# Optimization experiments

Measured on AMD Instinct MI355X. Metric: run time of the kernel, lower is better.

Reference implementation:

```python
import math
import jax, jax.numpy as jnp
import numpy as np

V_NODES = 100000
N_EDGES = 1600000
EMBED = 768
HID = 256
H = 4
FH = HID // H
L = 2
PE_D = EMBED // 4  # 192
SLOPE = 0.2


def make_pe(max_len, d):
    pos = np.arange(max_len, dtype=np.float32)[:, None]
    div = np.exp(np.arange(0, d, 2, dtype=np.float32) * (-math.log(10000.0) / d))
    pe = np.zeros((max_len, d), dtype=np.float32)
    pe[:, 0::2] = np.sin(pos * div)
    pe[:, 1::2] = np.cos(pos * div)
    return jnp.asarray(pe)


def setup_inputs() -> dict:
    key = jax.random.key(0)
    ks = jax.random.split(key, 24)

    def xavier(k, shape):
        fan_in, fan_out = shape[0], shape[1]
        lim = math.sqrt(6.0 / (fan_in + fan_out))
        return jax.random.uniform(k, shape, jnp.float32, -lim, lim)

    in_proj_dim = EMBED + 2 * PE_D  # 1152
    inp = {
        'row_idx': jax.random.randint(ks[0], (V_NODES,), 0, 256),
        'col_idx': jax.random.randint(ks[1], (V_NODES,), 0, 64),
        'edge_index': jax.random.randint(ks[2], (2, N_EDGES), 0, V_NODES),
        'edge_weight': jax.random.uniform(ks[3], (N_EDGES,), jnp.float32),
        'W_in': xavier(ks[4], (in_proj_dim, HID)),
        'b_in': jnp.zeros((HID,), jnp.float32),
        'ln_g': jnp.ones((HID,), jnp.float32),
        'ln_b': jnp.zeros((HID,), jnp.float32),
        'Wq': jnp.stack([xavier(ks[5 + i], (HID, HID)) for i in range(L)]),
        'bq': jnp.zeros((L, HID), jnp.float32),
        'Wk': jnp.stack([xavier(ks[7 + i], (HID, HID)) for i in range(L)]),
        'bk': jnp.zeros((L, HID), jnp.float32),
        'Wv': jnp.stack([xavier(ks[9 + i], (HID, HID)) for i in range(L)]),
        'bv': jnp.zeros((L, HID), jnp.float32),
        'Wo': jnp.stack([xavier(ks[11 + i], (HID, HID)) for i in range(L)]),
        'bo': jnp.zeros((L, HID), jnp.float32),
        'We': jnp.stack([xavier(ks[13 + i], (1, H)) for i in range(L)]),  # edge_proj weight [1,H]
        'be': jnp.zeros((L, H), jnp.float32),
    }
    return inp


def gat_layer(h, src, tgt, ew, Wq, bq, Wk, bk, Wv, bv, Wo, bo, We, be):
    V = h.shape[0]
    Q = (h @ Wq + bq).reshape(V, H, FH)
    K = (h @ Wk + bk).reshape(V, H, FH)
    Vo = (h @ Wv + bv).reshape(V, H, FH)
    # edge bias: Linear(1,H) on edge_weight, then leaky relu -> [E,H]
    edge_bias = jax.nn.leaky_relu(ew[:, None] * We.reshape(1, H) + be, SLOPE)
    attn_raw = jnp.sum(Q[src] * K[tgt], axis=-1) / math.sqrt(FH) + edge_bias  # [E,H]
    attn_exp = jnp.exp(attn_raw)
    deg = jax.ops.segment_sum(attn_exp, tgt, num_segments=V) + 1e-16  # [V,H]
    attn_norm = attn_exp / deg[tgt]  # [E,H] (dropout is identity at eval)
    msg = Vo[src] * attn_norm[:, :, None] * ew[:, None, None]  # [E,H,FH]
    out = jax.ops.segment_sum(msg, tgt, num_segments=V).reshape(V, H * FH)
    return jax.nn.leaky_relu(out @ Wo + bo, SLOPE)


def reference(row_idx, col_idx, edge_index, edge_weight,
              W_in, b_in, ln_g, ln_b,
              Wq, bq, Wk, bk, Wv, bv, Wo, bo, We, be):
    V = row_idx.shape[0]
    row_pe = make_pe(256, PE_D)
    col_pe = make_pe(64, PE_D)
    cell = jnp.zeros((V, EMBED), jnp.float32)  # cell_embeds are zeros in source
    h = jnp.concatenate([cell, row_pe[row_idx], col_pe[col_idx]], axis=-1)
    # input_proj: Linear -> LayerNorm -> ReLU (dropout identity)
    h = h @ W_in + b_in
    mu = jnp.mean(h, axis=-1, keepdims=True)
    var = jnp.var(h, axis=-1, keepdims=True)
    h = (h - mu) / jnp.sqrt(var + 1e-5) * ln_g + ln_b
    h = jax.nn.relu(h)
    src, tgt = edge_index[0], edge_index[1]
    for i in range(L):
        h = gat_layer(h, src, tgt, edge_weight,
                      Wq[i], bq[i], Wk[i], bk[i], Wv[i], bv[i],
                      Wo[i], bo[i], We[i], be[i])
    return h
```

## Files before the change

### kernel.cpp

```cpp
#include <hip/hip_runtime.h>
#include <hip/hip_bf16.h>
#include <type_traits>
#include <math.h>

typedef __attribute__((ext_vector_type(8))) short bf16x8;
typedef __attribute__((ext_vector_type(4))) float f32x4;

typedef __attribute__((address_space(3))) char       lds_char;
typedef const __attribute__((address_space(1))) char g_char;

__device__ __forceinline__ float bf2f(unsigned int u16) {
    union { unsigned int i; float f; } x; x.i = (u16 & 0xffffu) << 16; return x.f;
}
__device__ __forceinline__ unsigned int f2bf(float f) {
    union { float f; unsigned int i; } x; x.f = f;
    unsigned int i = x.i;
    unsigned int r = i + 0x7fffu + ((i >> 16) & 1u);
    return r >> 16;
}

#define SLOPE 0.2f

__global__ void k_hist(const int* __restrict__ tgt, int* __restrict__ cnt, int E) {
    int i = blockIdx.x * blockDim.x + threadIdx.x;
    if (i < E) atomicAdd(&cnt[tgt[i]], 1);
}

__global__ void __launch_bounds__(1024) k_scan1(const int* __restrict__ in, int* __restrict__ out,
                                                int* __restrict__ bsums, int n) {
    __shared__ int sm[1024];
    int i = blockIdx.x * 1024 + threadIdx.x;
    int v = (i < n) ? in[i] : 0;
    sm[threadIdx.x] = v; __syncthreads();
    for (int ofs = 1; ofs < 1024; ofs <<= 1) {
        int t = (threadIdx.x >= ofs) ? sm[threadIdx.x - ofs] : 0;
        __syncthreads();
        sm[threadIdx.x] += t;
        __syncthreads();
    }
    if (i < n) out[i] = sm[threadIdx.x];
    if (threadIdx.x == 1023) bsums[blockIdx.x] = sm[1023];
}

__global__ void __launch_bounds__(1024) k_scan2(int* bsums, int nb) {
    __shared__ int sm[1024];
    int v = (threadIdx.x < nb) ? bsums[threadIdx.x] : 0;
    sm[threadIdx.x] = v; __syncthreads();
    for (int ofs = 1; ofs < 1024; ofs <<= 1) {
        int t = (threadIdx.x >= ofs) ? sm[threadIdx.x - ofs] : 0;
        __syncthreads();
        sm[threadIdx.x] += t;
        __syncthreads();
    }
    if (threadIdx.x < nb) bsums[threadIdx.x] = sm[threadIdx.x] - v;
}

__global__ void __launch_bounds__(1024) k_scan3(int* __restrict__ out1, const int* __restrict__ bsums,
                                                int* __restrict__ off0, int n) {
    int i = blockIdx.x * 1024 + threadIdx.x;
    if (i < n) out1[i] += bsums[blockIdx.x];
    if (i == 0) off0[0] = 0;
}

__global__ void k_scatter(const int* __restrict__ ei, const float* __restrict__ ew,
                          const int* __restrict__ off, int* __restrict__ fill,
                          int2* __restrict__ p, int E) {
    int e = blockIdx.x * blockDim.x + threadIdx.x;
    if (e < E) {
        int s = ei[e], t = ei[E + e];
        int pos = off[t] + atomicAdd(&fill[t], 1);
        p[pos] = make_int2(s, __float_as_int(ew[e]));
    }
}

__global__ void __launch_bounds__(256) k_prep(const float* __restrict__ Wq, const float* __restrict__ Wk,
                                              const float* __restrict__ Wv, const float* __restrict__ Wo,
                                              unsigned short* __restrict__ WT,
                                              const float* __restrict__ bq, const float* __restrict__ bk,
                                              const float* __restrict__ bv, const float* __restrict__ bo,
                                              float* __restrict__ biasF,
                                              const float* __restrict__ W_in, float* __restrict__ AB,
                                              const int* __restrict__ ri, const int* __restrict__ ci,
                                              int* __restrict__ combo, int V) {
    __shared__ float sm[64][65];
    int blk = blockIdx.x;
    int tid = threadIdx.x;
    if (blk < 128) {
        int m = blk >> 4, t = blk & 15;
        int tr = t >> 2, tc = t & 3;
        const float* srcs[4] = {Wq, Wk, Wv, Wo};
        const float* W = srcs[m & 3] + (size_t)(m >> 2) * 65536;
        for (int i = tid; i < 4096; i += 256) {
            int r = i >> 6, c = i & 63;
            sm[r][c] = W[(size_t)(tr * 64 + r) * 256 + tc * 64 + c];
        }
        __syncthreads();
        for (int i = tid; i < 4096; i += 256) {
            int n = i >> 6, k = i & 63;
            WT[(size_t)(m * 256 + tc * 64 + n) * 256 + tr * 64 + k] = (unsigned short)f2bf(sm[k][n]);
        }
    } else if (blk < 136) {
        int m = blk - 128;
        const float* srcs[4] = {bq, bk, bv, bo};
        biasF[m * 256 + tid] = srcs[m & 3][(m >> 2) * 256 + tid];
    } else if (blk < 456) {
        int b2 = blk - 136;
        bool isA = b2 < 256;
        int pos = isA ? b2 : b2 - 256;
        const float* Wb = W_in + (size_t)(isA ? 768 : 960) * 256;
        float* pe = &sm[0][0];
        if (tid < 192) {
            float div = expf(-(float)(tid & ~1) * (logf(10000.0f) / 192.0f));
            float ang = (float)pos * div;
            pe[tid] = (tid & 1) ? cosf(ang) : sinf(ang);
        }
        __syncthreads();
        float acc = 0.f;
        #pragma unroll 8
        for (int d = 0; d < 192; ++d) acc = fmaf(pe[d], Wb[d * 256 + tid], acc);
        AB[b2 * 256 + tid] = acc;
    } else {
        int v = (blk - 456) * 256 + tid;
        if (v < V) combo[v] = ri[v] * 64 + ci[v];
    }
}

__global__ void __launch_bounds__(256) k_h0(const float* __restrict__ AB, const float* __restrict__ b_in,
                                            const float* __restrict__ g, const float* __restrict__ b,
                                            unsigned short* __restrict__ h0t) {
    int wid = threadIdx.x >> 6, lane = threadIdx.x & 63;
    int m = blockIdx.x * 4 + wid;
    int r = m >> 6, c = m & 63;
    float4 a  = ((const float4*)(AB + (size_t)r * 256))[lane];
    float4 bb = ((const float4*)(AB + (size_t)(256 + c) * 256))[lane];
    float4 bi = ((const float4*)b_in)[lane];
    float x0 = a.x + bb.x + bi.x, x1 = a.y + bb.y + bi.y;
    float x2 = a.z + bb.z + bi.z, x3 = a.w + bb.w + bi.w;
    float s = x0 + x1 + x2 + x3;
    #pragma unroll
    for (int msk = 1; msk < 64; msk <<= 1) s += __shfl_xor(s, msk);
    float mu = s * (1.f / 256.f);
    float d0 = x0 - mu, d1 = x1 - mu, d2 = x2 - mu, d3 = x3 - mu;
    float sq = d0 * d0 + d1 * d1 + d2 * d2 + d3 * d3;
    #pragma unroll
    for (int msk = 1; msk < 64; msk <<= 1) sq += __shfl_xor(sq, msk);
    float rstd = rsqrtf(sq * (1.f / 256.f) + 1e-5f);
    float4 gv = ((const float4*)g)[lane], bv = ((const float4*)b)[lane];
    float y0 = fmaxf(fmaf(d0 * rstd, gv.x, bv.x), 0.f);
    float y1 = fmaxf(fmaf(d1 * rstd, gv.y, bv.y), 0.f);
    float y2 = fmaxf(fmaf(d2 * rstd, gv.z, bv.z), 0.f);
    float y3 = fmaxf(fmaf(d3 * rstd, gv.w, bv.w), 0.f);
    uint2 o;
    o.x = f2bf(y0) | (f2bf(y1) << 16);
    o.y = f2bf(y2) | (f2bf(y3) << 16);
    *(uint2*)(h0t + (size_t)m * 256 + lane * 4) = o;
}

template <typename TC, bool LEAKY>
__global__ void __launch_bounds__(256) k_mm(const unsigned short* __restrict__ A,
                                            const unsigned short* __restrict__ WT,
                                            const float* __restrict__ bias,
                                            TC* __restrict__ C, int M, int ldc) {
    __shared__ __align__(16) char AsB[16384];
    __shared__ __align__(16) char BsB[16384];
    int tid = threadIdx.x;
    int R0 = blockIdx.x * 128, C0 = blockIdx.y * 128;
    int lane = tid & 63, wave = tid >> 6;
    int wr = (wave >> 1) * 64, wc = (wave & 1) * 64;
    int fr = lane & 15, fq = lane >> 4;
    f32x4 acc[4][4] = {};
    for (int k0 = 0; k0 < 256; k0 += 64) {
        #pragma unroll
        for (int it = 0; it < 4; ++it) {
            int chunk = it * 256 + tid;
            int r = chunk >> 3, cb = (chunk & 7) * 16;
            int sc = cb ^ ((r & 7) << 4);
            int gr = R0 + r;
            if (gr < M)
                __builtin_amdgcn_global_load_lds(
                    (g_char*)((const char*)(A + (size_t)gr * 256 + k0) + sc),
                    (lds_char*)(AsB + (size_t)(it * 256 + wave * 64) * 16), 16, 0, 0);
            __builtin_amdgcn_global_load_lds(
                (g_char*)((const char*)(WT + (size_t)(C0 + r) * 256 + k0) + sc),
                (lds_char*)(BsB + (size_t)(it * 256 + wave * 64) * 16), 16, 0, 0);
        }
        __syncthreads();
        #pragma unroll
        for (int ks = 0; ks < 2; ++ks) {
            bf16x8 af[4], bfv[4];
            #pragma unroll
            for (int mi = 0; mi < 4; ++mi) {
                int r = wr + mi * 16 + fr;
                int kb = ks * 64 + fq * 16;
                af[mi] = *(const bf16x8*)(AsB + r * 128 + (kb ^ ((r & 7) << 4)));
            }
            #pragma unroll
            for (int ni = 0; ni < 4; ++ni) {
                int r = wc + ni * 16 + fr;
                int kb = ks * 64 + fq * 16;
                bfv[ni] = *(const bf16x8*)(BsB + r * 128 + (kb ^ ((r & 7) << 4)));
            }
            #pragma unroll
            for (int mi = 0; mi < 4; ++mi)
                #pragma unroll
                for (int ni = 0; ni < 4; ++ni)
                    acc[mi][ni] = __builtin_amdgcn_mfma_f32_16x16x32_bf16(af[mi], bfv[ni], acc[mi][ni], 0, 0, 0);
        }
        __syncthreads();
    }
    #pragma unroll
    for (int mi = 0; mi < 4; ++mi) {
        #pragma unroll
        for (int r = 0; r < 4; ++r) {
            int row = R0 + wr + mi * 16 + fq * 4 + r;
            if (row >= M) continue;
            #pragma unroll
            for (int ni = 0; ni < 4; ++ni) {
                int col = C0 + wc + ni * 16 + fr;
                float v = acc[mi][ni][r] + bias[col];
                if (LEAKY) v = fmaxf(v, SLOPE * v);
                if constexpr (std::is_same<TC, float>::value) {
                    C[(size_t)row * ldc + col] = v;
                } else {
                    C[(size_t)row * ldc + col] = (unsigned short)f2bf(v);
                }
            }
        }
    }
}

template <bool USE_COMBO>
__global__ void __launch_bounds__(256) k_edge(const int* __restrict__ off, const int2* __restrict__ pedge,
                                              const int* __restrict__ combo,
                                              const unsigned short* __restrict__ QKV,
                                              const float* __restrict__ We_l, const float* __restrict__ be_l,
                                              unsigned short* __restrict__ out, int V) {
    int wid = threadIdx.x >> 6, lane = threadIdx.x & 63;
    int t = blockIdx.x * 4 + wid;
    if (t >= V) return;
    int q = lane & 15, quarter = lane >> 4;
    int h = q >> 2;
    int krow = USE_COMBO ? combo[t] : t;
    uint4 ka = *(const uint4*)(QKV + (size_t)krow * 768 + 256 + q * 16);
    uint4 kb = *(const uint4*)(QKV + (size_t)krow * 768 + 256 + q * 16 + 8);
    float kf[16];
    kf[0] = bf2f(ka.x); kf[1] = bf2f(ka.x >> 16); kf[2] = bf2f(ka.y); kf[3] = bf2f(ka.y >> 16);
    kf[4] = bf2f(ka.z); kf[5] = bf2f(ka.z >> 16); kf[6] = bf2f(ka.w); kf[7] = bf2f(ka.w >> 16);
    kf[8] = bf2f(kb.x); kf[9] = bf2f(kb.x >> 16); kf[10] = bf2f(kb.y); kf[11] = bf2f(kb.y >> 16);
    kf[12] = bf2f(kb.z); kf[13] = bf2f(kb.z >> 16); kf[14] = bf2f(kb.w); kf[15] = bf2f(kb.w >> 16);
    float Weh = We_l[h], beh = be_l[h];
    float n[16];
    #pragma unroll
    for (int j = 0; j < 16; ++j) n[j] = 0.f;
    float den = 0.f;
    int beg = off[t], end = off[t + 1];
    for (int e0 = beg; e0 < end; e0 += 64) {
        int nrem = end - e0; if (nrem > 64) nrem = 64;
        int sv = 0; float wv = 0.f;
        if (lane < nrem) {
            int2 pr = pedge[e0 + lane];
            sv = pr.x;
            wv = __int_as_float(pr.y);
            if (USE_COMBO) sv = combo[sv];
        }
        for (int i = 0; i < nrem; i += 4) {
            int ei = i + quarter;
            bool act = ei < nrem;
            int eidx = act ? ei : (nrem - 1);
            int srow = __shfl(sv, eidx);
            float w  = __shfl(wv, eidx);
            const unsigned short* base = QKV + (size_t)srow * 768 + q * 16;
            uint4 qa = *(const uint4*)base;
            uint4 qb = *(const uint4*)(base + 8);
            uint4 va = *(const uint4*)(base + 512);
            uint4 vb = *(const uint4*)(base + 520);
            float p;
            p = bf2f(qa.x) * kf[0];
            p = fmaf(bf2f(qa.x >> 16), kf[1], p);
            p = fmaf(bf2f(qa.y),       kf[2], p);
            p = fmaf(bf2f(qa.y >> 16), kf[3], p);
            p = fmaf(bf2f(qa.z),       kf[4], p);
            p = fmaf(bf2f(qa.z >> 16), kf[5], p);
            p = fmaf(bf2f(qa.w),       kf[6], p);
            p = fmaf(bf2f(qa.w >> 16), kf[7], p);
            p = fmaf(bf2f(qb.x),       kf[8], p);
            p = fmaf(bf2f(qb.x >> 16), kf[9], p);
            p = fmaf(bf2f(qb.y),       kf[10], p);
            p = fmaf(bf2f(qb.y >> 16), kf[11], p);
            p = fmaf(bf2f(qb.z),       kf[12], p);
            p = fmaf(bf2f(qb.z >> 16), kf[13], p);
            p = fmaf(bf2f(qb.w),       kf[14], p);
            p = fmaf(bf2f(qb.w >> 16), kf[15], p);
            p += __shfl_xor(p, 1);
            p += __shfl_xor(p, 2);
            float bias = fmaf(w, Weh, beh);
            bias = fmaxf(bias, SLOPE * bias);
            float ex = act ? __expf(fmaf(p, 0.125f, bias)) : 0.f;
            den += ex;
            float cc = ex * w;
            n[0]  = fmaf(cc, bf2f(va.x),       n[0]);
            n[1]  = fmaf(cc, bf2f(va.x >> 16), n[1]);
            n[2]  = fmaf(cc, bf2f(va.y),       n[2]);
            n[3]  = fmaf(cc, bf2f(va.y >> 16), n[3]);
            n[4]  = fmaf(cc, bf2f(va.z),       n[4]);
            n[5]  = fmaf(cc, bf2f(va.z >> 16), n[5]);
            n[6]  = fmaf(cc, bf2f(va.w),       n[6]);
            n[7]  = fmaf(cc, bf2f(va.w >> 16), n[7]);
            n[8]  = fmaf(cc, bf2f(vb.x),       n[8]);
            n[9]  = fmaf(cc, bf2f(vb.x >> 16), n[9]);
            n[10] = fmaf(cc, bf2f(vb.y),       n[10]);
            n[11] = fmaf(cc, bf2f(vb.y >> 16), n[11]);
            n[12] = fmaf(cc, bf2f(vb.z),       n[12]);
            n[13] = fmaf(cc, bf2f(vb.z >> 16), n[13]);
            n[14] = fmaf(cc, bf2f(vb.w),       n[14]);
            n[15] = fmaf(cc, bf2f(vb.w >> 16), n[15]);
        }
    }
    den += __shfl_xor(den, 16);
    den += __shfl_xor(den, 32);
    #pragma unroll
    for (int j = 0; j < 16; ++j) {
        n[j] += __shfl_xor(n[j], 16);
        n[j] += __shfl_xor(n[j], 32);
    }
    float inv = 1.f / (den + 1e-16f);
    if (quarter == 0) {
        uint4 o0, o1;
        o0.x = f2bf(n[0] * inv)  | (f2bf(n[1] * inv) << 16);
        o0.y = f2bf(n[2] * inv)  | (f2bf(n[3] * inv) << 16);
        o0.z = f2bf(n[4] * inv)  | (f2bf(n[5] * inv) << 16);
        o0.w = f2bf(n[6] * inv)  | (f2bf(n[7] * inv) << 16);
        o1.x = f2bf(n[8] * inv)  | (f2bf(n[9] * inv) << 16);
        o1.y = f2bf(n[10] * inv) | (f2bf(n[11] * inv) << 16);
        o1.z = f2bf(n[12] * inv) | (f2bf(n[13] * inv) << 16);
        o1.w = f2bf(n[14] * inv) | (f2bf(n[15] * inv) << 16);
        *(uint4*)(out + (size_t)t * 256 + q * 16) = o0;
        *(uint4*)(out + (size_t)t * 256 + q * 16 + 8) = o1;
    }
}

extern "C" void kernel_launch(void* const* d_in, const int* in_sizes, int n_in,
                              void* d_out, int out_size, void* d_ws, size_t ws_size,
                              hipStream_t stream) {
    const int*   row_idx = (const int*)d_in[0];
    const int*   col_idx = (const int*)d_in[1];
    const int*   ei      = (const int*)d_in[2];
    const float* ew      = (const float*)d_in[3];
    const float* W_in    = (const float*)d_in[4];
    const float* b_in    = (const float*)d_in[5];
    const float* ln_g    = (const float*)d_in[6];
    const float* ln_b    = (const float*)d_in[7];
    const float* Wq      = (const float*)d_in[8];
    const float* bq      = (const float*)d_in[9];
    const float* Wk      = (const float*)d_in[10];
    const float* bk      = (const float*)d_in[11];
    const float* Wv      = (const float*)d_in[12];
    const float* bv      = (const float*)d_in[13];
    const float* Wo      = (const float*)d_in[14];
    const float* bo      = (const float*)d_in[15];
    const float* We      = (const float*)d_in[16];
    const float* be      = (const float*)d_in[17];

    const int V = in_sizes[0];
    const int E = in_sizes[3];
    const int NC = 16384;

    char* w = (char*)d_ws;
    size_t o = 0;
    auto alloc = [&](size_t bytes) -> char* {
        char* p = w + o;
        o = (o + bytes + 255) & ~(size_t)255;
        return p;
    };
    int*   cnt     = (int*)alloc((size_t)V * 4);
    int*   fill    = (int*)alloc((size_t)V * 4);
    int*   csr_off = (int*)alloc((size_t)(V + 1) * 4);
    int*   bsums   = (int*)alloc(1024 * 4);
    int2*  csrP    = (int2*)alloc((size_t)E * 8);
    int*   combo   = (int*)alloc((size_t)V * 4);
    float* AB      = (float*)alloc((size_t)320 * 256 * 4);
    unsigned short* WT    = (unsigned short*)alloc((size_t)2048 * 256 * 2);
    float*          biasF = (float*)alloc((size_t)2048 * 4);
    unsigned short* h0t   = (unsigned short*)alloc((size_t)NC * 256 * 2);
    unsigned short* QKV1  = (unsigned short*)alloc((size_t)NC * 768 * 2);
    unsigned short* out_e = (unsigned short*)alloc((size_t)V * 256 * 2);
    unsigned short* h1    = (unsigned short*)alloc((size_t)V * 256 * 2);
    unsigned short* QKV2  = (unsigned short*)alloc((size_t)V * 768 * 2);

    hipMemsetAsync(cnt, 0, (size_t)2 * V * 4 + 256, stream);

    int eb = (E + 255) / 256;
    int nscan = (V + 1023) / 1024;
    int prep_blocks = 456 + (V + 255) / 256;
    k_prep<<<prep_blocks, 256, 0, stream>>>(Wq, Wk, Wv, Wo, WT, bq, bk, bv, bo, biasF,
                                            W_in, AB, row_idx, col_idx, combo, V);
    k_hist<<<eb, 256, 0, stream>>>(ei + E, cnt, E);
    k_scan1<<<nscan, 1024, 0, stream>>>(cnt, csr_off + 1, bsums, V);
    k_scan2<<<1, 1024, 0, stream>>>(bsums, nscan);
    k_scan3<<<nscan, 1024, 0, stream>>>(csr_off + 1, bsums, csr_off, V);
    k_scatter<<<eb, 256, 0, stream>>>(ei, ew, csr_off, fill, csrP, E);

    k_h0<<<NC / 4, 256, 0, stream>>>(AB, b_in, ln_g, ln_b, h0t);

    dim3 g1(NC / 128, 6);
    k_mm<unsigned short, false><<<g1, 256, 0, stream>>>(h0t, WT, biasF, QKV1, NC, 768);

    int tb = (V + 3) / 4;
    k_edge<true><<<tb, 256, 0, stream>>>(csr_off, csrP, combo, QKV1, We, be, out_e, V);

    int mb = (V + 127) / 128;
    dim3 go(mb, 2);
    dim3 gqkv(mb, 6);
    k_mm<unsigned short, true><<<go, 256, 0, stream>>>(out_e, WT + (size_t)768 * 256, biasF + 768, h1, V, 256);
    k_mm<unsigned short, false><<<gqkv, 256, 0, stream>>>(h1, WT + (size_t)1024 * 256, biasF + 1024, QKV2, V, 768);

    k_edge<false><<<tb, 256, 0, stream>>>(csr_off, csrP, combo, QKV2, We + 4, be + 4, out_e, V);

    k_mm<float, true><<<go, 256, 0, stream>>>(out_e, WT + (size_t)1792 * 256, biasF + 1792, (float*)d_out, V, 256);
}
```

Baseline: 777.1 us.

## Store layer-1 QKV head-major and split first edge kernel per head

```diff
diff --git a/kernel.cpp b/kernel.cpp
--- a/kernel.cpp
+++ b/kernel.cpp
@@ -156,11 +156,11 @@
     *(uint2*)(h0t + (size_t)m * 256 + lane * 4) = o;
 }
 
-template <typename TC, bool LEAKY>
+template <typename TC, bool LEAKY, bool PERM>
 __global__ void __launch_bounds__(256) k_mm(const unsigned short* __restrict__ A,
                                             const unsigned short* __restrict__ WT,
                                             const float* __restrict__ bias,
-                                            TC* __restrict__ C, int M, int ldc) {
+                                            TC* __restrict__ C, int M, int ldc, int permN) {
     __shared__ __align__(16) char AsB[16384];
     __shared__ __align__(16) char BsB[16384];
     int tid = threadIdx.x;
@@ -219,7 +219,11 @@
                 int col = C0 + wc + ni * 16 + fr;
                 float v = acc[mi][ni][r] + bias[col];
                 if (LEAKY) v = fmaxf(v, SLOPE * v);
-                if constexpr (std::is_same<TC, float>::value) {
+                if constexpr (PERM) {
+                    int part = col >> 8, hh = (col & 255) >> 6, f = col & 63;
+                    size_t addr = (((size_t)hh * permN + row) * 192) + part * 64 + f;
+                    C[addr] = (TC)f2bf(v);
+                } else if constexpr (std::is_same<TC, float>::value) {
                     C[(size_t)row * ldc + col] = v;
                 } else {
                     C[(size_t)row * ldc + col] = (unsigned short)f2bf(v);
@@ -229,9 +233,91 @@
     }
 }
 
-template <bool USE_COMBO>
+__global__ void __launch_bounds__(256) k_edge1h(const int* __restrict__ off, const int2* __restrict__ pedge,
+                                                const int* __restrict__ combo,
+                                                const unsigned short* __restrict__ T1,
+                                                const float* __restrict__ We_l, const float* __restrict__ be_l,
+                                                unsigned short* __restrict__ out, int V, int NC) {
+    int wid = threadIdx.x >> 6, lane = threadIdx.x & 63;
+    int t = blockIdx.x * 4 + wid;
+    int h = blockIdx.y;
+    if (t >= V) return;
+    int g = lane >> 3, l = lane & 7;
+    int krow = combo[t];
+    const unsigned short* Tbase = T1 + (size_t)h * NC * 192;
+    uint4 ku = *(const uint4*)(Tbase + (size_t)krow * 192 + 64 + l * 8);
+    float kf[8];
+    kf[0] = bf2f(ku.x); kf[1] = bf2f(ku.x >> 16); kf[2] = bf2f(ku.y); kf[3] = bf2f(ku.y >> 16);
+    kf[4] = bf2f(ku.z); kf[5] = bf2f(ku.z >> 16); kf[6] = bf2f(ku.w); kf[7] = bf2f(ku.w >> 16);
+    float Weh = We_l[h], beh = be_l[h];
+    float n[8] = {0.f, 0.f, 0.f, 0.f, 0.f, 0.f, 0.f, 0.f};
+    float den = 0.f;
+    int beg = off[t], end = off[t + 1];
+    for (int e0 = beg; e0 < end; e0 += 64) {
+        int nrem = end - e0; if (nrem > 64) nrem = 64;
+        int sv = 0; float wv = 0.f;
+        if (lane < nrem) {
+            int2 pr = pedge[e0 + lane];
+            sv = combo[pr.x];
+            wv = __int_as_float(pr.y);
+        }
+        for (int i = 0; i < nrem; i += 8) {
+            int ei = i + g;
+            bool act = ei < nrem;
+            int eidx = act ? ei : (nrem - 1);
+            int srow = __shfl(sv, eidx);
+            float w  = __shfl(wv, eidx);
+            const unsigned short* qb = Tbase + (size_t)srow * 192 + l * 8;
+            uint4 qa = *(const uint4*)qb;
+            uint4 va = *(const uint4*)(qb + 128);
+            float p;
+            p = bf2f(qa.x) * kf[0];
+            p = fmaf(bf2f(qa.x >> 16), kf[1], p);
+            p = fmaf(bf2f(qa.y),       kf[2], p);
+            p = fmaf(bf2f(qa.y >> 16), kf[3], p);
+            p = fmaf(bf2f(qa.z),       kf[4], p);
+            p = fmaf(bf2f(qa.z >> 16), kf[5], p);
+            p = fmaf(bf2f(qa.w),       kf[6], p);
+            p = fmaf(bf2f(qa.w >> 16), kf[7], p);
+            p += __shfl_xor(p, 1);
+            p += __shfl_xor(p, 2);
+            p += __shfl_xor(p, 4);
+            float bias = fmaf(w, Weh, beh);
+            bias = fmaxf(bias, SLOPE * bias);
+            float ex = act ? __expf(fmaf(p, 0.125f, bias)) : 0.f;
+            den += ex;
+            float cc = ex * w;
+            n[0] = fmaf(cc, bf2f(va.x),       n[0]);
+            n[1] = fmaf(cc, bf2f(va.x >> 16), n[1]);
+            n[2] = fmaf(cc, bf2f(va.y),       n[2]);
+            n[3] = fmaf(cc, bf2f(va.y >> 16), n[3]);
+            n[4] = fmaf(cc, bf2f(va.z),       n[4]);
+            n[5] = fmaf(cc, bf2f(va.z >> 16), n[5]);
+            n[6] = fmaf(cc, bf2f(va.w),       n[6]);
+            n[7] = fmaf(cc, bf2f(va.w >> 16), n[7]);
+        }
+    }
+    den += __shfl_xor(den, 8);
+    den += __shfl_xor(den, 16);
+    den += __shfl_xor(den, 32);
+    #pragma unroll
+    for (int j = 0; j < 8; ++j) {
+        n[j] += __shfl_xor(n[j], 8);
+        n[j] += __shfl_xor(n[j], 16);
+        n[j] += __shfl_xor(n[j], 32);
+    }
+    float inv = 1.f / (den + 1e-16f);
+    if (g == 0) {
+        uint4 o;
+        o.x = f2bf(n[0] * inv) | (f2bf(n[1] * inv) << 16);
+        o.y = f2bf(n[2] * inv) | (f2bf(n[3] * inv) << 16);
+        o.z = f2bf(n[4] * inv) | (f2bf(n[5] * inv) << 16);
+        o.w = f2bf(n[6] * inv) | (f2bf(n[7] * inv) << 16);
+        *(uint4*)(out + (size_t)t * 256 + h * 64 + l * 8) = o;
+    }
+}
+
 __global__ void __launch_bounds__(256) k_edge(const int* __restrict__ off, const int2* __restrict__ pedge,
-                                              const int* __restrict__ combo,
                                               const unsigned short* __restrict__ QKV,
                                               const float* __restrict__ We_l, const float* __restrict__ be_l,
                                               unsigned short* __restrict__ out, int V) {
@@ -240,9 +326,8 @@
     if (t >= V) return;
     int q = lane & 15, quarter = lane >> 4;
     int h = q >> 2;
-    int krow = USE_COMBO ? combo[t] : t;
-    uint4 ka = *(const uint4*)(QKV + (size_t)krow * 768 + 256 + q * 16);
-    uint4 kb = *(const uint4*)(QKV + (size_t)krow * 768 + 256 + q * 16 + 8);
+    uint4 ka = *(const uint4*)(QKV + (size_t)t * 768 + 256 + q * 16);
+    uint4 kb = *(const uint4*)(QKV + (size_t)t * 768 + 256 + q * 16 + 8);
     float kf[16];
     kf[0] = bf2f(ka.x); kf[1] = bf2f(ka.x >> 16); kf[2] = bf2f(ka.y); kf[3] = bf2f(ka.y >> 16);
     kf[4] = bf2f(ka.z); kf[5] = bf2f(ka.z >> 16); kf[6] = bf2f(ka.w); kf[7] = bf2f(ka.w >> 16);
@@ -261,7 +346,6 @@
             int2 pr = pedge[e0 + lane];
             sv = pr.x;
             wv = __int_as_float(pr.y);
-            if (USE_COMBO) sv = combo[sv];
         }
         for (int i = 0; i < nrem; i += 4) {
             int ei = i + quarter;
@@ -382,7 +466,7 @@
     unsigned short* WT    = (unsigned short*)alloc((size_t)2048 * 256 * 2);
     float*          biasF = (float*)alloc((size_t)2048 * 4);
     unsigned short* h0t   = (unsigned short*)alloc((size_t)NC * 256 * 2);
-    unsigned short* QKV1  = (unsigned short*)alloc((size_t)NC * 768 * 2);
+    unsigned short* T1    = (unsigned short*)alloc((size_t)4 * NC * 192 * 2);
     unsigned short* out_e = (unsigned short*)alloc((size_t)V * 256 * 2);
     unsigned short* h1    = (unsigned short*)alloc((size_t)V * 256 * 2);
     unsigned short* QKV2  = (unsigned short*)alloc((size_t)V * 768 * 2);
@@ -403,18 +487,19 @@
     k_h0<<<NC / 4, 256, 0, stream>>>(AB, b_in, ln_g, ln_b, h0t);
 
     dim3 g1(NC / 128, 6);
-    k_mm<unsigned short, false><<<g1, 256, 0, stream>>>(h0t, WT, biasF, QKV1, NC, 768);
+    k_mm<unsigned short, false, true><<<g1, 256, 0, stream>>>(h0t, WT, biasF, T1, NC, 768, NC);
 
     int tb = (V + 3) / 4;
-    k_edge<true><<<tb, 256, 0, stream>>>(csr_off, csrP, combo, QKV1, We, be, out_e, V);
+    dim3 ge1(tb, 4);
+    k_edge1h<<<ge1, 256, 0, stream>>>(csr_off, csrP, combo, T1, We, be, out_e, V, NC);
 
     int mb = (V + 127) / 128;
     dim3 go(mb, 2);
     dim3 gqkv(mb, 6);
-    k_mm<unsigned short, true><<<go, 256, 0, stream>>>(out_e, WT + (size_t)768 * 256, biasF + 768, h1, V, 256);
-    k_mm<unsigned short, false><<<gqkv, 256, 0, stream>>>(h1, WT + (size_t)1024 * 256, biasF + 1024, QKV2, V, 768);
-
-    k_edge<false><<<tb, 256, 0, stream>>>(csr_off, csrP, combo, QKV2, We + 4, be + 4, out_e, V);
-
-    k_mm<float, true><<<go, 256, 0, stream>>>(out_e, WT + (size_t)1792 * 256, biasF + 1792, (float*)d_out, V, 256);
-}
+    k_mm<unsigned short, true, false><<<go, 256, 0, stream>>>(out_e, WT + (size_t)768 * 256, biasF + 768, h1, V, 256, 0);
+    k_mm<unsigned short, false, false><<<gqkv, 256, 0, stream>>>(h1, WT + (size_t)1024 * 256, biasF + 1024, QKV2, V, 768, 0);
+
+    k_edge<<<tb, 256, 0, stream>>>(csr_off, csrP, QKV2, We + 4, be + 4, out_e, V);
+
+    k_mm<float, true, false><<<go, 256, 0, stream>>>(out_e, WT + (size_t)1792 * 256, biasF + 1792, (float*)d_out, V, 256, 0);
+}
```

Result: no change. 791.2 us (+1.8%).
